# Kernel optimization log

Hardware: AMD Instinct MI355X
Metric: run time of the kernel (lower is better)

Reference implementation:

```python
import jax, jax.numpy as jnp
import numpy as np

DIM = 1024
SCALE_DIM = 4
QK_DIM = DIM // SCALE_DIM  # 256
B, S = 4, 4096


def setup_inputs() -> dict:
    key = jax.random.key(0)
    ks = jax.random.split(key, 8)
    std = 1.0 / np.sqrt(DIM)  # keep activations O(1)
    return {
        "q": jax.random.normal(ks[0], (B, S, DIM), jnp.float32),
        "k": jax.random.normal(ks[1], (B, S, DIM), jnp.float32),
        "v": jax.random.normal(ks[2], (B, S, DIM), jnp.float32),
        "Wq": jax.random.normal(ks[3], (QK_DIM, DIM), jnp.float32) * std,
        "bq": jnp.zeros((QK_DIM,), jnp.float32),
        "Wk": jax.random.normal(ks[4], (QK_DIM, DIM), jnp.float32) * std,
        "bk": jnp.zeros((QK_DIM,), jnp.float32),
        "Wv": jax.random.normal(ks[5], (DIM, DIM), jnp.float32) * std,
        "bv": jnp.zeros((DIM,), jnp.float32),
    }


def reference(q, k, v, Wq, bq, Wk, bk, Wv, bv):
    scale = jnp.asarray(np.sqrt(QK_DIM), q.dtype)
    qp = jnp.einsum("bsd,ed->bse", q, Wq) + bq  # [B,S,QK_DIM]
    kp = jnp.einsum("bsd,ed->bse", k, Wk) + bk  # [B,S,QK_DIM]
    vp = jnp.einsum("bsd,ed->bse", v, Wv) + bv  # [B,S,DIM]
    z = jnp.einsum("bqe,bke->bqk", qp, kp)      # [B,S,S]
    z = jax.nn.sigmoid(z / scale)
    return jnp.einsum("bqk,bkd->bqd", z, vp)     # [B,S,DIM]
```

## Files before the change

kernel.cpp:

```cpp
#include <hip/hip_runtime.h>
#include <cstdint>
#include <cstddef>


typedef __bf16 bf16;
typedef __bf16 v8bf __attribute__((ext_vector_type(8)));
typedef __bf16 v4bf __attribute__((ext_vector_type(4)));
typedef float  v16f __attribute__((ext_vector_type(16)));
typedef float  v4f  __attribute__((ext_vector_type(4)));

#define DIMV  1024
#define QKD   256
#define BATCH 4
#define SEQ   4096

#define TM 128
#define TN 128
#define BK 32

__global__ __launch_bounds__(256) void cast_f32_bf16(const float* __restrict__ in,
                                                     bf16* __restrict__ out, int n4) {
  int i = blockIdx.x * 256 + threadIdx.x;
  if (i >= n4) return;
  const float4 v = reinterpret_cast<const float4*>(in)[i];
  v4bf o;
  o[0] = (bf16)v.x; o[1] = (bf16)v.y; o[2] = (bf16)v.z; o[3] = (bf16)v.w;
  reinterpret_cast<v4bf*>(out)[i] = o;
}

__device__ __forceinline__ void gload_lds16(const void* g, void* l) {
  __builtin_amdgcn_global_load_lds((const __attribute__((address_space(1))) void*)g,
                                   (__attribute__((address_space(3))) void*)l,
                                   16, 0, 0);
}

template <int MODE>
__global__ __launch_bounds__(256) void gemm_nt(
    const bf16* __restrict__ A, long As_z,
    const bf16* __restrict__ B, long Bs_z,
    const float* __restrict__ bias0, const float* __restrict__ bias1,
    void* __restrict__ Cv, long Cs_z,
    int K, int lda, int ldb, int ldc) {
  __shared__ __align__(16) bf16 As[TM * BK];
  __shared__ __align__(16) bf16 Bs[TN * BK];
  const int tid  = threadIdx.x;
  const int wave = tid >> 6;
  const int lane = tid & 63;
  const int zb   = blockIdx.z;
  A = A + (size_t)zb * As_z;
  B = B + (size_t)zb * Bs_z;
  const float* bias = (MODE == 0 && zb) ? bias1 : bias0;

  const int row0 = blockIdx.x * TM;
  const int col0 = blockIdx.y * TN;
  const int wm = (wave & 1) * 64;
  const int wn = (wave >> 1) * 64;
  const int l31  = lane & 31;
  const int half = lane >> 5;

  v16f acc[2][2] = {};

  const char* gA = (const char*)A;
  const char* gB = (const char*)B;
  const size_t sA = (size_t)lda * 2;
  const size_t sB = (size_t)ldb * 2;

  const int row_s = tid >> 2;
  const int qg    = (tid & 3) ^ ((row_s >> 1) & 3);
  const int kb    = qg * 16;
  char* ldsA = (char*)As + wave * 1024;
  char* ldsB = (char*)Bs + wave * 1024;

  const char* pa0 = gA + (size_t)(row0 + row_s) * sA + kb;
  const char* pa1 = gA + (size_t)(row0 + row_s + 64) * sA + kb;
  const char* pb0 = gB + (size_t)(col0 + row_s) * sB + kb;
  const char* pb1 = gB + (size_t)(col0 + row_s + 64) * sB + kb;

  const int swz  = (lane >> 1) & 3;
  const int off0 = (half ^ swz) * 8;
  const int off1 = off0 ^ 16;
  const int raA0 = (wm + l31) * BK,      raA1 = (wm + 32 + l31) * BK;
  const int raB0 = (wn + l31) * BK,      raB1 = (wn + 32 + l31) * BK;

  const int kIters = K / BK;
  for (int kt = 0; kt < kIters; ++kt) {
    gload_lds16(pa0, ldsA);
    gload_lds16(pa1, ldsA + 4096);
    gload_lds16(pb0, ldsB);
    gload_lds16(pb1, ldsB + 4096);
    pa0 += BK * 2; pa1 += BK * 2; pb0 += BK * 2; pb1 += BK * 2;
    __syncthreads();

    v8bf a[2][2], b[2][2];
    a[0][0] = *(const v8bf*)&As[raA0 + off0];
    a[0][1] = *(const v8bf*)&As[raA0 + off1];
    a[1][0] = *(const v8bf*)&As[raA1 + off0];
    a[1][1] = *(const v8bf*)&As[raA1 + off1];
    b[0][0] = *(const v8bf*)&Bs[raB0 + off0];
    b[0][1] = *(const v8bf*)&Bs[raB0 + off1];
    b[1][0] = *(const v8bf*)&Bs[raB1 + off0];
    b[1][1] = *(const v8bf*)&Bs[raB1 + off1];
#pragma unroll
    for (int kk = 0; kk < 2; ++kk)
#pragma unroll
      for (int i = 0; i < 2; ++i)
#pragma unroll
        for (int j = 0; j < 2; ++j)
          acc[i][j] = __builtin_amdgcn_mfma_f32_32x32x16_bf16(a[i][kk], b[j][kk], acc[i][j], 0, 0, 0);
    __syncthreads();
  }

#pragma unroll
  for (int i = 0; i < 2; ++i) {
    const int rb = row0 + wm + i * 32 + 4 * half;
#pragma unroll
    for (int j = 0; j < 2; ++j) {
      const int gcol = col0 + wn + j * 32 + l31;
      float badd = 0.f;
      if (MODE == 0 || MODE == 1) badd = bias[gcol];
      if (MODE == 1) {
        const int b = rb >> 12;
        bf16* cb = &((bf16*)Cv)[((size_t)(b * DIMV + gcol)) * SEQ];
        const int s0 = rb & 4095;
#pragma unroll
        for (int blk = 0; blk < 4; ++blk) {
          v4bf o;
#pragma unroll
          for (int rr = 0; rr < 4; ++rr) o[rr] = (bf16)(acc[i][j][4 * blk + rr] + badd);
          *(v4bf*)&cb[s0 + 8 * blk] = o;
        }
      } else {
#pragma unroll
        for (int blk = 0; blk < 4; ++blk)
#pragma unroll
          for (int rr = 0; rr < 4; ++rr) {
            const int grow = rb + 8 * blk + rr;
            float v = acc[i][j][4 * blk + rr];
            if (MODE == 0) {
              ((bf16*)Cv)[(size_t)zb * Cs_z + (size_t)grow * ldc + gcol] = (bf16)(v + badd);
            } else if (MODE == 2) {
              v = 1.f / (1.f + __expf(v * -0.0625f));
              ((bf16*)Cv)[(size_t)zb * Cs_z + (size_t)grow * ldc + gcol] = (bf16)v;
            } else {
              ((float*)Cv)[(size_t)zb * Cs_z + (size_t)grow * ldc + gcol] = v;
            }
          }
      }
    }
  }
}

#define FENCE() asm volatile("" ::: "memory")
#define BAR8()  do { FENCE(); __builtin_amdgcn_s_barrier(); FENCE(); } while (0)
#define WAIT_LGKM0() asm volatile("s_waitcnt lgkmcnt(0)" ::: "memory")
#define WAIT_VM6()   asm volatile("s_waitcnt vmcnt(6)" ::: "memory")
#define WAIT_VM0()   asm volatile("s_waitcnt vmcnt(0)" ::: "memory")

template <int MODE>
__global__ __launch_bounds__(512, 2) void gemm_nt8(
    const bf16* __restrict__ A, long As_z,
    const bf16* __restrict__ B, long Bs_z,
    const float* __restrict__ bias0,
    void* __restrict__ Cv, long Cs_z,
    int K, int lda, int ldb, int ldc) {
  __shared__ __align__(16) bf16 lds[2][4][8192];
  char* ldsBase = (char*)&lds[0][0][0];
  const int tid = threadIdx.x;
  const int w   = tid >> 6;
  const int l   = tid & 63;
  const int zb  = blockIdx.z;
  A += (size_t)zb * As_z;
  B += (size_t)zb * Bs_z;

  const int row0 = blockIdx.x * 256;
  const int col0 = blockIdx.y * 256;
  const int wmi  = w >> 2;
  const int wni  = w & 3;
  const int l4 = l & 15, lh = l >> 4;

  const int rsub = l >> 3;
  const int cg   = (l & 7) ^ rsub;
  const size_t sA = (size_t)lda * 2, sB = (size_t)ldb * 2;
  const size_t sA64 = sA * 64, sB64 = sB * 64;
  const char* pA0 = (const char*)A + (size_t)(row0 +       w * 8 + rsub) * sA + cg * 16;
  const char* pA1 = (const char*)A + (size_t)(row0 + 128 + w * 8 + rsub) * sA + cg * 16;
  const char* pB0 = (const char*)B + (size_t)(col0 +       w * 8 + rsub) * sB + cg * 16;
  const char* pB1 = (const char*)B + (size_t)(col0 + 128 + w * 8 + rsub) * sB + cg * 16;
  const int wq = w * 1024;

  const int off0 = l4 * 128 + ((lh ^ (l & 7)) << 4);
  const int off1 = off0 ^ 64;

  v4f acc[8][4] = {};

#define STAGE_K(ptr, sec, d, s64)                                   \
  do {                                                              \
    char* _lb = ldsBase + (d) * 65536 + (sec) * 16384 + wq;         \
    gload_lds16(ptr, _lb);                                          \
    gload_lds16((ptr) + (s64), _lb + 8192);                         \
    (ptr) += 128;                                                   \
  } while (0)

#define READ_A(MOFF)                                                         \
  _Pragma("unroll") for (int mm = 0; mm < 4; ++mm) {                         \
    a_[mm][0] = *(const v8bf*)(aB + ((MOFF) + mm) * 2048 + off0);            \
    a_[mm][1] = *(const v8bf*)(aB + ((MOFF) + mm) * 2048 + off1);            \
  }
#define READ_B()                                                             \
  _Pragma("unroll") for (int nn = 0; nn < 4; ++nn) {                         \
    b_[nn][0] = *(const v8bf*)(bB + nn * 2048 + off0);                       \
    b_[nn][1] = *(const v8bf*)(bB + nn * 2048 + off1);                       \
  }
#define MFMA_Q(M0, N0)                                                       \
  _Pragma("unroll") for (int mm = 0; mm < 4; ++mm)                           \
  _Pragma("unroll") for (int nn = 0; nn < 2; ++nn)                           \
  _Pragma("unroll") for (int kk = 0; kk < 2; ++kk)                           \
    acc[(M0) + mm][(N0) + nn] = __builtin_amdgcn_mfma_f32_16x16x32_bf16(     \
        a_[mm][kk], b_[(N0) + nn][kk], acc[(M0) + mm][(N0) + nn], 0, 0, 0);

  const int nt = K >> 6;

  STAGE_K(pB0, 2, 0, sB64);
  STAGE_K(pB1, 3, 0, sB64);
  STAGE_K(pA0, 0, 0, sA64);
  STAGE_K(pA1, 1, 0, sA64);
  STAGE_K(pB0, 2, 1, sB64);
  STAGE_K(pB1, 3, 1, sB64);
  STAGE_K(pA0, 0, 1, sA64);
  WAIT_VM6();
  BAR8();

  v8bf a_[4][2], b_[4][2];

  for (int t = 0; t < nt - 1; ++t) {
    const int d  = t & 1;
    const int dn = d ^ 1;
    const char* aB = ldsBase + d * 65536 + wmi * 16384;
    const char* bB = ldsBase + d * 65536 + 32768 + (wni >> 1) * 16384 + (wni & 1) * 8192;
    const bool pf = (t < nt - 2);
    READ_A(0);
    READ_B();
    STAGE_K(pA1, 1, dn, sA64);
    BAR8();
    WAIT_LGKM0();
    __builtin_amdgcn_s_setprio(1);
    MFMA_Q(0, 0);
    __builtin_amdgcn_s_setprio(0);
    BAR8();
    if (pf) STAGE_K(pB0, 2, d, sB64);
    BAR8();
    WAIT_LGKM0();
    __builtin_amdgcn_s_setprio(1);
    MFMA_Q(0, 2);
    __builtin_amdgcn_s_setprio(0);
    BAR8();
    READ_A(4);
    if (pf) STAGE_K(pB1, 3, d, sB64);
    BAR8();
    WAIT_LGKM0();
    __builtin_amdgcn_s_setprio(1);
    MFMA_Q(4, 0);
    __builtin_amdgcn_s_setprio(0);
    BAR8();
    if (pf) STAGE_K(pA0, 0, d, sA64);
    BAR8();
    WAIT_LGKM0();
    __builtin_amdgcn_s_setprio(1);
    MFMA_Q(4, 2);
    __builtin_amdgcn_s_setprio(0);
    if (pf) WAIT_VM6(); else WAIT_VM0();
    BAR8();
  }
  {
    const int d = (nt - 1) & 1;
    const char* aB = ldsBase + d * 65536 + wmi * 16384;
    const char* bB = ldsBase + d * 65536 + 32768 + (wni >> 1) * 16384 + (wni & 1) * 8192;
    READ_A(0);
    READ_B();
    MFMA_Q(0, 0);
    MFMA_Q(0, 2);
    READ_A(4);
    MFMA_Q(4, 0);
    MFMA_Q(4, 2);
  }

  const int rbase = row0 + wmi * 128 + 4 * lh;
#pragma unroll
  for (int mm = 0; mm < 8; ++mm) {
    const int rb = rbase + mm * 16;
#pragma unroll
    for (int nn = 0; nn < 4; ++nn) {
      const int gcol = col0 + wni * 64 + nn * 16 + l4;
      if (MODE == 1) {
        const int b = rb >> 12;
        bf16* cb = &((bf16*)Cv)[((size_t)(b * DIMV + gcol)) * SEQ];
        const int s0 = rb & 4095;
        const float badd = bias0[gcol];
        v4bf o;
#pragma unroll
        for (int rr = 0; rr < 4; ++rr) o[rr] = (bf16)(acc[mm][nn][rr] + badd);
        *(v4bf*)&cb[s0] = o;
      } else if (MODE == 2) {
#pragma unroll
        for (int rr = 0; rr < 4; ++rr) {
          float v = acc[mm][nn][rr];
          v = 1.f / (1.f + __expf(v * -0.0625f));
          ((bf16*)Cv)[(size_t)zb * Cs_z + (size_t)(rb + rr) * ldc + gcol] = (bf16)v;
        }
      } else {
#pragma unroll
        for (int rr = 0; rr < 4; ++rr)
          ((float*)Cv)[(size_t)zb * Cs_z + (size_t)(rb + rr) * ldc + gcol] = acc[mm][nn][rr];
      }
    }
  }
#undef STAGE_K
#undef READ_A
#undef READ_B
#undef MFMA_Q
}

extern "C" void kernel_launch(void* const* d_in, const int* in_sizes, int n_in,
                              void* d_out, int out_size, void* d_ws, size_t ws_size,
                              hipStream_t stream) {
  const float* q  = (const float*)d_in[0];
  const float* k  = (const float*)d_in[1];
  const float* v  = (const float*)d_in[2];
  const float* Wq = (const float*)d_in[3];
  const float* bq = (const float*)d_in[4];
  const float* Wk = (const float*)d_in[5];
  const float* bk = (const float*)d_in[6];
  const float* Wv = (const float*)d_in[7];
  const float* bv = (const float*)d_in[8];
  float* out = (float*)d_out;

  const size_t MB = 1024 * 1024;
  char* ws = (char*)d_ws;

  int g;
  size_t zcap;
  if (ws_size >= 188 * MB)      { g = 4; zcap = 128 * MB; }
  else if (ws_size >= 121 * MB) { g = 2; zcap = 64 * MB; }
  else                          { g = 1; zcap = 64 * MB; }

  bf16 *castA, *castB, *zbuf, *Wq16, *Wk16, *Wv16, *qp16, *kp16, *vpT;
  if (g >= 2) {
    castA = (bf16*)ws;
    castB = (bf16*)(ws + 32 * MB);
    zbuf  = (bf16*)ws;
    char* p = ws + zcap;
    Wq16 = (bf16*)p;             p += 524288;
    Wk16 = (bf16*)p;             p += 524288;
    Wv16 = (bf16*)p;             p += 2097152;
    qp16 = (bf16*)p;             p += 8388608;
    kp16 = (bf16*)p;             p += 8388608;
    vpT  = (bf16*)p;
  } else {
    castA = (bf16*)ws;
    zbuf  = castA;
    char* p = ws + 32 * MB;
    Wq16 = (bf16*)p;             p += 524288;
    Wk16 = (bf16*)p;             p += 524288;
    Wv16 = (bf16*)p;             p += 2097152;
    qp16 = (bf16*)p;             p += 8388608;
    kp16 = (bf16*)p;             p += 8388608;
    vpT  = (bf16*)p;
    castB = vpT;
  }

  const int NQKV = BATCH * SEQ * DIMV;

  auto cast = [&](const float* src, bf16* dst, int n) {
    int n4 = n / 4;
    cast_f32_bf16<<<dim3((n4 + 255) / 256), dim3(256), 0, stream>>>(src, dst, n4);
  };

  cast(Wq, Wq16, QKD * DIMV);
  cast(Wk, Wk16, QKD * DIMV);
  cast(Wv, Wv16, DIMV * DIMV);
  cast(q, castA, NQKV);
  cast(k, castB, NQKV);

  gemm_nt<0><<<dim3(BATCH * SEQ / TM, QKD / TN, 2), dim3(256), 0, stream>>>(
      castA, (long)(castB - castA), Wq16, (long)(QKD * DIMV), bq, bk,
      qp16, (long)(kp16 - qp16), DIMV, DIMV, DIMV, QKD);

  cast(v, castA, NQKV);
  gemm_nt8<1><<<dim3(BATCH * SEQ / 256, DIMV / 256, 1), dim3(512), 0, stream>>>(
      castA, 0L, Wv16, 0L, bv,
      vpT, 0L, DIMV, DIMV, DIMV, 0);

  const long zstride = (long)SEQ * SEQ;
  for (int ig = 0; ig < BATCH / g; ++ig) {
    const size_t b0 = (size_t)ig * g;
    gemm_nt8<2><<<dim3(SEQ / 256, SEQ / 256, g), dim3(512), 0, stream>>>(
        qp16 + b0 * SEQ * QKD, (long)(SEQ * QKD),
        kp16 + b0 * SEQ * QKD, (long)(SEQ * QKD),
        nullptr, zbuf, zstride, QKD, QKD, QKD, SEQ);
    gemm_nt8<3><<<dim3(SEQ / 256, DIMV / 256, g), dim3(512), 0, stream>>>(
        zbuf, zstride, vpT + b0 * DIMV * SEQ, (long)(DIMV * SEQ),
        nullptr, out + b0 * SEQ * DIMV, (long)(SEQ * DIMV),
        SEQ, SEQ, SEQ, DIMV);
  }
}
```

Before: 473.2 us.

## Fuse f32-to-bf16 cast into Q/K projection, remap workgroups, regroup B staging

The Q and K projection GEMM now reads fp32 activations directly, converts them to bf16 in registers and writes them to LDS. This removes two separate full-size cast kernels and their bf16 intermediate round trip through memory. The 8-wave GEMM also remaps block IDs into a strided order, likely to improve cache locality across XCDs, and issues both B staging loads in the same phase. The trade-off is that the projection kernel loses its async global-to-LDS path for A and now does synchronous fp32 loads with conversion.

```diff
diff --git a/kernel.cpp b/kernel.cpp
--- a/kernel.cpp
+++ b/kernel.cpp
@@ -34,12 +34,11 @@
                                    16, 0, 0);
 }
 
-template <int MODE>
-__global__ __launch_bounds__(256) void gemm_nt(
-    const bf16* __restrict__ A, long As_z,
+__global__ __launch_bounds__(256) void gemm_proj(
+    const float* __restrict__ A0f, const float* __restrict__ A1f,
     const bf16* __restrict__ B, long Bs_z,
     const float* __restrict__ bias0, const float* __restrict__ bias1,
-    void* __restrict__ Cv, long Cs_z,
+    bf16* __restrict__ Cv, long Cs_z,
     int K, int lda, int ldb, int ldc) {
   __shared__ __align__(16) bf16 As[TM * BK];
   __shared__ __align__(16) bf16 Bs[TN * BK];
@@ -47,9 +46,9 @@
   const int wave = tid >> 6;
   const int lane = tid & 63;
   const int zb   = blockIdx.z;
-  A = A + (size_t)zb * As_z;
+  const float* Af = zb ? A1f : A0f;
   B = B + (size_t)zb * Bs_z;
-  const float* bias = (MODE == 0 && zb) ? bias1 : bias0;
+  const float* bias = zb ? bias1 : bias0;
 
   const int row0 = blockIdx.x * TM;
   const int col0 = blockIdx.y * TN;
@@ -60,21 +59,18 @@
 
   v16f acc[2][2] = {};
 
-  const char* gA = (const char*)A;
-  const char* gB = (const char*)B;
-  const size_t sA = (size_t)lda * 2;
   const size_t sB = (size_t)ldb * 2;
 
   const int row_s = tid >> 2;
   const int qg    = (tid & 3) ^ ((row_s >> 1) & 3);
-  const int kb    = qg * 16;
-  char* ldsA = (char*)As + wave * 1024;
+
+  const float* fa0 = Af + (size_t)(row0 + row_s) * lda + qg * 8;
+  const float* fa1 = fa0 + (size_t)64 * lda;
+  const char*  pb0 = (const char*)B + (size_t)(col0 + row_s) * sB + qg * 16;
+  const char*  pb1 = pb0 + 64 * sB;
   char* ldsB = (char*)Bs + wave * 1024;
-
-  const char* pa0 = gA + (size_t)(row0 + row_s) * sA + kb;
-  const char* pa1 = gA + (size_t)(row0 + row_s + 64) * sA + kb;
-  const char* pb0 = gB + (size_t)(col0 + row_s) * sB + kb;
-  const char* pb1 = gB + (size_t)(col0 + row_s + 64) * sB + kb;
+  char* wA0  = (char*)As + tid * 16;
+  char* wA1  = wA0 + 4096;
 
   const int swz  = (lane >> 1) & 3;
   const int off0 = (half ^ swz) * 8;
@@ -84,11 +80,20 @@
 
   const int kIters = K / BK;
   for (int kt = 0; kt < kIters; ++kt) {
-    gload_lds16(pa0, ldsA);
-    gload_lds16(pa1, ldsA + 4096);
+    const float4 x00 = *(const float4*)(fa0);
+    const float4 x01 = *(const float4*)(fa0 + 4);
+    const float4 x10 = *(const float4*)(fa1);
+    const float4 x11 = *(const float4*)(fa1 + 4);
     gload_lds16(pb0, ldsB);
     gload_lds16(pb1, ldsB + 4096);
-    pa0 += BK * 2; pa1 += BK * 2; pb0 += BK * 2; pb1 += BK * 2;
+    fa0 += BK; fa1 += BK; pb0 += BK * 2; pb1 += BK * 2;
+    v8bf w0, w1;
+    w0[0]=(bf16)x00.x; w0[1]=(bf16)x00.y; w0[2]=(bf16)x00.z; w0[3]=(bf16)x00.w;
+    w0[4]=(bf16)x01.x; w0[5]=(bf16)x01.y; w0[6]=(bf16)x01.z; w0[7]=(bf16)x01.w;
+    w1[0]=(bf16)x10.x; w1[1]=(bf16)x10.y; w1[2]=(bf16)x10.z; w1[3]=(bf16)x10.w;
+    w1[4]=(bf16)x11.x; w1[5]=(bf16)x11.y; w1[6]=(bf16)x11.z; w1[7]=(bf16)x11.w;
+    *(v8bf*)wA0 = w0;
+    *(v8bf*)wA1 = w1;
     __syncthreads();
 
     v8bf a[2][2], b[2][2];
@@ -116,36 +121,15 @@
 #pragma unroll
     for (int j = 0; j < 2; ++j) {
       const int gcol = col0 + wn + j * 32 + l31;
-      float badd = 0.f;
-      if (MODE == 0 || MODE == 1) badd = bias[gcol];
-      if (MODE == 1) {
-        const int b = rb >> 12;
-        bf16* cb = &((bf16*)Cv)[((size_t)(b * DIMV + gcol)) * SEQ];
-        const int s0 = rb & 4095;
-#pragma unroll
-        for (int blk = 0; blk < 4; ++blk) {
-          v4bf o;
-#pragma unroll
-          for (int rr = 0; rr < 4; ++rr) o[rr] = (bf16)(acc[i][j][4 * blk + rr] + badd);
-          *(v4bf*)&cb[s0 + 8 * blk] = o;
+      const float badd = bias[gcol];
+#pragma unroll
+      for (int blk = 0; blk < 4; ++blk)
+#pragma unroll
+        for (int rr = 0; rr < 4; ++rr) {
+          const int grow = rb + 8 * blk + rr;
+          Cv[(size_t)zb * Cs_z + (size_t)grow * ldc + gcol] =
+              (bf16)(acc[i][j][4 * blk + rr] + badd);
         }
-      } else {
-#pragma unroll
-        for (int blk = 0; blk < 4; ++blk)
-#pragma unroll
-          for (int rr = 0; rr < 4; ++rr) {
-            const int grow = rb + 8 * blk + rr;
-            float v = acc[i][j][4 * blk + rr];
-            if (MODE == 0) {
-              ((bf16*)Cv)[(size_t)zb * Cs_z + (size_t)grow * ldc + gcol] = (bf16)(v + badd);
-            } else if (MODE == 2) {
-              v = 1.f / (1.f + __expf(v * -0.0625f));
-              ((bf16*)Cv)[(size_t)zb * Cs_z + (size_t)grow * ldc + gcol] = (bf16)v;
-            } else {
-              ((float*)Cv)[(size_t)zb * Cs_z + (size_t)grow * ldc + gcol] = v;
-            }
-          }
-      }
     }
   }
 }
@@ -172,8 +156,14 @@
   A += (size_t)zb * As_z;
   B += (size_t)zb * Bs_z;
 
-  const int row0 = blockIdx.x * 256;
-  const int col0 = blockIdx.y * 256;
+  const int NX = gridDim.x, NY = gridDim.y;
+  const int nwg = NX * NY;
+  const int d_id = blockIdx.x + NX * blockIdx.y;
+  const int L = (d_id & 7) * (nwg >> 3) + (d_id >> 3);
+  const int lx = L / NY, ly = L % NY;
+
+  const int row0 = lx * 256;
+  const int col0 = ly * 256;
   const int wmi  = w >> 2;
   const int wni  = w & 3;
   const int l4 = l & 15, lh = l >> 4;
@@ -247,7 +237,7 @@
     MFMA_Q(0, 0);
     __builtin_amdgcn_s_setprio(0);
     BAR8();
-    if (pf) STAGE_K(pB0, 2, d, sB64);
+    if (pf) { STAGE_K(pB0, 2, d, sB64); STAGE_K(pB1, 3, d, sB64); }
     BAR8();
     WAIT_LGKM0();
     __builtin_amdgcn_s_setprio(1);
@@ -255,7 +245,6 @@
     __builtin_amdgcn_s_setprio(0);
     BAR8();
     READ_A(4);
-    if (pf) STAGE_K(pB1, 3, d, sB64);
     BAR8();
     WAIT_LGKM0();
     __builtin_amdgcn_s_setprio(1);
@@ -343,10 +332,9 @@
   else if (ws_size >= 121 * MB) { g = 2; zcap = 64 * MB; }
   else                          { g = 1; zcap = 64 * MB; }
 
-  bf16 *castA, *castB, *zbuf, *Wq16, *Wk16, *Wv16, *qp16, *kp16, *vpT;
+  bf16 *castA, *zbuf, *Wq16, *Wk16, *Wv16, *qp16, *kp16, *vpT;
   if (g >= 2) {
     castA = (bf16*)ws;
-    castB = (bf16*)(ws + 32 * MB);
     zbuf  = (bf16*)ws;
     char* p = ws + zcap;
     Wq16 = (bf16*)p;             p += 524288;
@@ -365,7 +353,6 @@
     qp16 = (bf16*)p;             p += 8388608;
     kp16 = (bf16*)p;             p += 8388608;
     vpT  = (bf16*)p;
-    castB = vpT;
   }
 
   const int NQKV = BATCH * SEQ * DIMV;
@@ -378,11 +365,9 @@
   cast(Wq, Wq16, QKD * DIMV);
   cast(Wk, Wk16, QKD * DIMV);
   cast(Wv, Wv16, DIMV * DIMV);
-  cast(q, castA, NQKV);
-  cast(k, castB, NQKV);
-
-  gemm_nt<0><<<dim3(BATCH * SEQ / TM, QKD / TN, 2), dim3(256), 0, stream>>>(
-      castA, (long)(castB - castA), Wq16, (long)(QKD * DIMV), bq, bk,
+
+  gemm_proj<<<dim3(BATCH * SEQ / TM, QKD / TN, 2), dim3(256), 0, stream>>>(
+      q, k, Wq16, (long)(QKD * DIMV), bq, bk,
       qp16, (long)(kp16 - qp16), DIMV, DIMV, DIMV, QKD);
 
   cast(v, castA, NQKV);
```

Measured after the change: 471.2 us. No clear change (-0.4%).
